# Kernel tuning notes

Measured on AMD Instinct MI355X. Metric: run time of the kernel, lower is better.

Reference implementation:

```python
import jax, jax.numpy as jnp
import numpy as np

H = 1024          # hidden_size
I = 4 * H         # intermediate_size
E = 8             # num routed experts
TOP_K = 2


def setup_inputs() -> dict:
    key = jax.random.key(0)
    ks = jax.random.split(key, 6)
    s = 0.02
    hidden_states = jax.random.normal(ks[0], (4, 4096, H), dtype=jnp.float32)
    # shared expert (num_shared_experts = 1)
    w1_shared = jax.random.normal(ks[1], (H, I), dtype=jnp.float32) * s  # up proj
    w2_shared = jax.random.normal(ks[2], (I, H), dtype=jnp.float32) * s  # down proj
    # routed experts stacked
    w1_routed = jax.random.normal(ks[3], (E, H, I), dtype=jnp.float32) * s
    w2_routed = jax.random.normal(ks[4], (E, I, H), dtype=jnp.float32) * s
    w_router = jax.random.normal(ks[5], (H, E), dtype=jnp.float32) * s
    return {
        "hidden_states": hidden_states,
        "w1_shared": w1_shared,
        "w2_shared": w2_shared,
        "w1_routed": w1_routed,
        "w2_routed": w2_routed,
        "w_router": w_router,
    }


def reference(hidden_states, w1_shared, w2_shared, w1_routed, w2_routed, w_router):
    bsz, seq_len, hidden_dim = hidden_states.shape
    flat = hidden_states.reshape(-1, hidden_dim)              # [T, H]

    # shared expert(s)
    shared_out = jax.nn.silu(flat @ w1_shared) @ w2_shared     # [T, H]

    # router -> softmax -> top-k -> renormalize
    router_logits = flat @ w_router                            # [T, E]
    routing_weights = jax.nn.softmax(router_logits, axis=-1)
    topk_w, topk_idx = jax.lax.top_k(routing_weights, TOP_K)   # [T, K]
    topk_w = topk_w / jnp.sum(topk_w, axis=-1, keepdims=True)

    # combine weights per expert: cw[t, e] = sum_k topk_w[t,k] * (topk_idx[t,k] == e)
    one_hot = jax.nn.one_hot(topk_idx, E, dtype=topk_w.dtype)  # [T, K, E]
    cw = jnp.einsum('tk,tke->te', topk_w, one_hot)             # [T, E]

    # per-expert dense MLP, weighted combine (zero weight == not routed)
    routed_out = jnp.zeros_like(flat)
    for e in range(E):  # fixed small loop over experts
        expert_out = jax.nn.silu(flat @ w1_routed[e]) @ w2_routed[e]  # [T, H]
        routed_out = routed_out + cw[:, e:e + 1] * expert_out

    total = shared_out + routed_out
    return total.reshape(bsz, seq_len, hidden_dim)
```

## Files before the change

kernel.cpp:

```cpp
#include <hip/hip_runtime.h>
#include <cmath>

typedef __bf16 bf16;
typedef bf16 bf16x4 __attribute__((ext_vector_type(4)));
typedef bf16 bf16x8 __attribute__((ext_vector_type(8)));
typedef float f32x4 __attribute__((ext_vector_type(4)));

#define T_TOK 16384
#define HD 1024
#define ID 4096
#define MAXR 51200

__device__ __forceinline__ void async16(const void* g, void* l) {
  void* gp = (void*)g;
  __builtin_amdgcn_global_load_lds((__attribute__((address_space(1))) void*)gp,
                                   (__attribute__((address_space(3))) void*)l,
                                   16, 0, 0);
}

__global__ __launch_bounds__(256)
void cast_x_kernel(const float* __restrict__ X, bf16* __restrict__ Xb) {
  const int i = (blockIdx.x * 256 + threadIdx.x) * 4;
  const float4 v = *(const float4*)(X + i);
  bf16x4 o;
  o.x = (bf16)v.x; o.y = (bf16)v.y; o.z = (bf16)v.z; o.w = (bf16)v.w;
  *(bf16x4*)(Xb + i) = o;
}

__global__ __launch_bounds__(256)
void transpose_cast(const float* __restrict__ srcR, const float* __restrict__ srcS,
                    bf16* __restrict__ dst, int R, int C) {
  const int e = blockIdx.z;
  const float* src = (e < 8) ? srcR + (size_t)e * R * C : srcS;
  __shared__ float tile[64][65];
  const int c0 = blockIdx.x * 64, r0 = blockIdx.y * 64;
  const int tx = threadIdx.x & 15;
  const int ty = threadIdx.x >> 4;
#pragma unroll
  for (int i = 0; i < 64; i += 16) {
    const float4 v = *(const float4*)(src + (size_t)(r0 + ty + i) * C + c0 + tx * 4);
    tile[ty + i][tx * 4 + 0] = v.x;
    tile[ty + i][tx * 4 + 1] = v.y;
    tile[ty + i][tx * 4 + 2] = v.z;
    tile[ty + i][tx * 4 + 3] = v.w;
  }
  __syncthreads();
  bf16* d = dst + (size_t)e * R * C;
#pragma unroll
  for (int i = 0; i < 64; i += 16) {
    const int col = ty + i;
    bf16x4 o;
    o.x = (bf16)tile[tx * 4 + 0][col];
    o.y = (bf16)tile[tx * 4 + 1][col];
    o.z = (bf16)tile[tx * 4 + 2][col];
    o.w = (bf16)tile[tx * 4 + 3][col];
    *(bf16x4*)(d + (size_t)(c0 + col) * R + r0 + tx * 4) = o;
  }
}

__global__ __launch_bounds__(1024)
void router_kernel(const float* __restrict__ X, const float* __restrict__ Wr,
                   int* __restrict__ topk_idx, float* __restrict__ topk_w) {
  __shared__ float W[1024 * 9];
  for (int i = threadIdx.x; i < 1024 * 8; i += 1024)
    W[(i >> 3) * 9 + (i & 7)] = Wr[i];
  __syncthreads();
  const int wave = threadIdx.x >> 6, lane = threadIdx.x & 63;
  const int t = blockIdx.x * 16 + wave;
  const float* xr = X + (size_t)t * HD;
  float acc[8] = {0.f, 0.f, 0.f, 0.f, 0.f, 0.f, 0.f, 0.f};
  for (int j = 0; j < 16; ++j) {
    const float x = xr[lane + j * 64];
    const float* wp = &W[(lane + j * 64) * 9];
#pragma unroll
    for (int e2 = 0; e2 < 8; ++e2) acc[e2] += x * wp[e2];
  }
#pragma unroll
  for (int off = 32; off; off >>= 1)
#pragma unroll
    for (int e2 = 0; e2 < 8; ++e2) acc[e2] += __shfl_down(acc[e2], off);
  if (lane == 0) {
    int i0 = 0; float m0 = acc[0];
#pragma unroll
    for (int e2 = 1; e2 < 8; ++e2) if (acc[e2] > m0) { m0 = acc[e2]; i0 = e2; }
    int i1 = -1; float m1 = -3.4e38f;
#pragma unroll
    for (int e2 = 0; e2 < 8; ++e2)
      if (e2 != i0 && acc[e2] > m1) { m1 = acc[e2]; i1 = e2; }
    const float w0 = 1.f / (1.f + __expf(m1 - m0));
    topk_idx[2 * t] = i0;  topk_idx[2 * t + 1] = i1;
    topk_w[2 * t] = w0;    topk_w[2 * t + 1] = 1.f - w0;
  }
}

__global__ __launch_bounds__(256)
void scatter_kernel(const int* __restrict__ topk_idx, const float* __restrict__ topk_w,
                    int* __restrict__ row_token, float* __restrict__ row_w,
                    int* __restrict__ row_exp, int* __restrict__ token_rows,
                    int* __restrict__ meta) {
  const int e = blockIdx.x;
  const int tid = threadIdx.x;
  __shared__ int hist[8];
  if (tid < 8) hist[tid] = 0;
  __syncthreads();
  for (int t = tid; t < T_TOK; t += 256) {
    atomicAdd(&hist[topk_idx[2 * t]], 1);
    atomicAdd(&hist[topk_idx[2 * t + 1]], 1);
  }
  __syncthreads();

  if (e == 8) {
    for (int r = tid; r < T_TOK; r += 256) {
      row_token[r] = r; row_w[r] = 1.f; row_exp[r] = 8;
    }
    if (tid == 0) {
      int tot = T_TOK;
      for (int i = 0; i < 8; ++i) tot += (hist[i] + 255) & ~255;
      meta[0] = tot;
    }
    return;
  }

  int base = T_TOK;
  for (int i = 0; i < e; ++i) base += (hist[i] + 255) & ~255;
  const int cnt = hist[e];
  const int pc = (cnt + 255) & ~255;

  __shared__ int wsum[4];
  const int wv = tid >> 6, ln = tid & 63;
  int written = 0;
  for (int c = 0; c < T_TOK / 256; ++c) {
    const int t = c * 256 + tid;
    const int i0 = topk_idx[2 * t], i1 = topk_idx[2 * t + 1];
    const int slot = (i0 == e) ? 0 : ((i1 == e) ? 1 : -1);
    const unsigned long long m = __ballot(slot >= 0);
    if (ln == 0) wsum[wv] = (int)__popcll(m);
    __syncthreads();
    int off = written;
    for (int i = 0; i < wv; ++i) off += wsum[i];
    if (slot >= 0) {
      const int rank = (int)__popcll(m & ((1ULL << ln) - 1ULL));
      const int pos = base + off + rank;
      row_token[pos] = t;
      row_w[pos] = topk_w[2 * t + slot];
      row_exp[pos] = e;
      token_rows[2 * t + slot] = pos;
    }
    written += wsum[0] + wsum[1] + wsum[2] + wsum[3];
    __syncthreads();
  }
  for (int p = written + tid; p < pc; p += 256) {
    row_token[base + p] = 0; row_w[base + p] = 0.f; row_exp[base + p] = e;
  }
}

template <int MODE, int NDIM, int KDIM>
__global__ __launch_bounds__(512)
void gemm8(const bf16* __restrict__ A0, const bf16* __restrict__ WT,
           bf16* __restrict__ bout, float* __restrict__ out,
           const int* __restrict__ row_token, const float* __restrict__ row_w,
           const int* __restrict__ row_exp, const int* __restrict__ meta,
           int range_start, int chunk_base) {
  constexpr int NT = KDIM / 32;
  const int total = meta[0];

  const int gx = gridDim.x;
  const int nwg = gx * gridDim.y;
  int id = blockIdx.y * gx + blockIdx.x;
  {
    const int q = nwg >> 3, rm = nwg & 7;
    const int xcd = id & 7, loc = id >> 3;
    id = (xcd < rm ? xcd * (q + 1) : rm * (q + 1) + (xcd - rm) * q) + loc;
  }
  const int bx = id % gx, by = id / gx;

  const int r0 = range_start + by * 256;
  if (r0 >= total) return;
  const int n0 = bx * 256;

  __shared__ __align__(16) char lds[3 * 32768];

  const int tid = threadIdx.x;
  const int wid = tid >> 6, lane = tid & 63;
  const int e = row_exp[r0];
  const bf16* W = WT + (size_t)e * NDIM * KDIM;

  const int tr = tid >> 2;
  const int tb = tid & 3;
  const int rA0 = tr, rA1 = tr + 128;
  const int bl0 = tb ^ ((rA0 >> 1) & 3);
  const int bl1 = tb ^ ((rA1 >> 1) & 3);
  const bf16 *gA0, *gA1;
  if (MODE == 0) {
    gA0 = A0 + (size_t)row_token[r0 + rA0] * KDIM + bl0 * 8;
    gA1 = A0 + (size_t)row_token[r0 + rA1] * KDIM + bl1 * 8;
  } else {
    gA0 = A0 + (size_t)(r0 - chunk_base + rA0) * KDIM + bl0 * 8;
    gA1 = A0 + (size_t)(r0 - chunk_base + rA1) * KDIM + bl1 * 8;
  }
  const bf16* gB0 = W + (size_t)(n0 + rA0) * KDIM + bl0 * 8;
  const bf16* gB1 = W + (size_t)(n0 + rA1) * KDIM + bl1 * 8;
  char* const ldsb = lds;
  const int wo = wid * 1024;

#define STAGE_A0(c, kt) async16(gA0 + (kt) * 32, ldsb + (c) * 32768 + wo)
#define STAGE_A1(c, kt) async16(gA1 + (kt) * 32, ldsb + (c) * 32768 + 8192 + wo)
#define STAGE_B0(c, kt) async16(gB0 + (kt) * 32, ldsb + (c) * 32768 + 16384 + wo)
#define STAGE_B1(c, kt) async16(gB1 + (kt) * 32, ldsb + (c) * 32768 + 24576 + wo)

  const int l15 = lane & 15, kg = lane >> 4;
  const int wr = wid >> 2, wc = wid & 3;
  int offA[8], offB[4];
#pragma unroll
  for (int m = 0; m < 8; ++m) {
    const int row = wr * 128 + m * 16 + l15;
    offA[m] = row * 64 + ((kg ^ ((row >> 1) & 3)) << 4);
  }
#pragma unroll
  for (int n = 0; n < 4; ++n) {
    const int row = wc * 64 + n * 16 + l15;
    offB[n] = 16384 + row * 64 + ((kg ^ ((row >> 1) & 3)) << 4);
  }

  f32x4 acc[8][4] = {};

  STAGE_A0(0, 0); STAGE_A1(0, 0); STAGE_B0(0, 0); STAGE_B1(0, 0);
  STAGE_A0(1, 1); STAGE_A1(1, 1); STAGE_B0(1, 1); STAGE_B1(1, 1);

  int cb = 0, cn = 2;
  for (int kt = 0; kt < NT; ++kt) {
    if (kt + 1 < NT) asm volatile("s_waitcnt vmcnt(4)" ::: "memory");
    else             asm volatile("s_waitcnt vmcnt(0)" ::: "memory");
    __builtin_amdgcn_s_barrier();
    asm volatile("" ::: "memory");
    __builtin_amdgcn_sched_barrier(0);
    const char* Tb = ldsb + cb * 32768;
    const bool pf = (kt + 2 < NT);
    const int k2 = kt + 2;
    bf16x8 bfr[4];
#pragma unroll
    for (int q = 0; q < 4; ++q) {
      if (pf) {
        if (q == 0)      STAGE_A0(cn, k2);
        else if (q == 1) STAGE_A1(cn, k2);
        else if (q == 2) STAGE_B0(cn, k2);
        else             STAGE_B1(cn, k2);
      }
      if (q == 0) {
#pragma unroll
        for (int n = 0; n < 4; ++n) bfr[n] = *(const bf16x8*)(Tb + offB[n]);
      }
      const bf16x8 a0 = *(const bf16x8*)(Tb + offA[2 * q]);
      const bf16x8 a1 = *(const bf16x8*)(Tb + offA[2 * q + 1]);
      __builtin_amdgcn_s_setprio(1);
#pragma unroll
      for (int n = 0; n < 4; ++n) {
        acc[2 * q][n] =
            __builtin_amdgcn_mfma_f32_16x16x32_bf16(a0, bfr[n], acc[2 * q][n], 0, 0, 0);
        acc[2 * q + 1][n] =
            __builtin_amdgcn_mfma_f32_16x16x32_bf16(a1, bfr[n], acc[2 * q + 1][n], 0, 0, 0);
      }
      __builtin_amdgcn_s_setprio(0);
    }
    cb = (cb == 2) ? 0 : cb + 1;
    cn = (cn == 2) ? 0 : cn + 1;
  }
#undef STAGE_A0
#undef STAGE_A1
#undef STAGE_B0
#undef STAGE_B1

  const int orow = wr * 128;
  const int ocol = n0 + wc * 64;
  if (MODE == 0) {
#pragma unroll
    for (int m = 0; m < 8; ++m) {
#pragma unroll
      for (int rr = 0; rr < 4; ++rr) {
        const int row = (r0 - chunk_base) + orow + m * 16 + kg * 4 + rr;
        bf16* p = bout + (size_t)row * NDIM + ocol + l15;
#pragma unroll
        for (int n = 0; n < 4; ++n) {
          const float x = acc[m][n][rr];
          p[n * 16] = (bf16)(x / (1.f + __expf(-x)));
        }
      }
    }
  } else if (e == 8) {
#pragma unroll
    for (int m = 0; m < 8; ++m) {
#pragma unroll
      for (int rr = 0; rr < 4; ++rr) {
        const int row = r0 + orow + m * 16 + kg * 4 + rr;
        const int tok = row_token[row];
        float* p = out + (size_t)tok * HD + ocol + l15;
#pragma unroll
        for (int n = 0; n < 4; ++n) p[n * 16] = acc[m][n][rr];
      }
    }
  } else {
#pragma unroll
    for (int m = 0; m < 8; ++m) {
#pragma unroll
      for (int rr = 0; rr < 4; ++rr) {
        const int row = r0 + orow + m * 16 + kg * 4 + rr;
        const float w = row_w[row];
        bf16* p = bout + (size_t)(row - T_TOK) * HD + ocol + l15;
#pragma unroll
        for (int n = 0; n < 4; ++n) p[n * 16] = (bf16)(w * acc[m][n][rr]);
      }
    }
  }
}

__global__ __launch_bounds__(256)
void combine_kernel(float* __restrict__ out, const bf16* __restrict__ routed_out,
                    const int* __restrict__ token_rows) {
  const int t = blockIdx.x;
  const int i = threadIdx.x * 4;
  const int rA = token_rows[2 * t] - T_TOK;
  const int rB = token_rows[2 * t + 1] - T_TOK;
  float4 o = *(const float4*)(out + (size_t)t * HD + i);
  const bf16x4 a = *(const bf16x4*)(routed_out + (size_t)rA * HD + i);
  const bf16x4 b = *(const bf16x4*)(routed_out + (size_t)rB * HD + i);
  o.x += (float)a.x + (float)b.x;
  o.y += (float)a.y + (float)b.y;
  o.z += (float)a.z + (float)b.z;
  o.w += (float)a.w + (float)b.w;
  *(float4*)(out + (size_t)t * HD + i) = o;
}

extern "C" void kernel_launch(void* const* d_in, const int* in_sizes, int n_in,
                              void* d_out, int out_size, void* d_ws, size_t ws_size,
                              hipStream_t stream) {
  const float* X   = (const float*)d_in[0];
  const float* w1s = (const float*)d_in[1];
  const float* w2s = (const float*)d_in[2];
  const float* w1r = (const float*)d_in[3];
  const float* w2r = (const float*)d_in[4];
  const float* wr  = (const float*)d_in[5];
  float* out = (float*)d_out;

  char* ws = (char*)d_ws;
  bf16* W1T       = (bf16*)(ws + 0);
  bf16* W2T       = (bf16*)(ws + 75497472);
  bf16* Xbf       = (bf16*)(ws + 150994944);
  int* topk_idx   = (int*)(ws + 184549376);
  float* topk_w   = (float*)(ws + 184680448);
  int* row_token  = (int*)(ws + 184811520);
  float* row_w    = (float*)(ws + 185016320);
  int* row_exp    = (int*)(ws + 185221120);
  int* token_rows = (int*)(ws + 185425920);
  int* meta       = (int*)(ws + 185556992);
  bf16* routed_out= (bf16*)(ws + 185557248);
  bf16* act       = (bf16*)(ws + 256860416);

  const size_t avail = ws_size - 256860416ULL;
  long long rc = (long long)(avail / (ID * 2));
  if (rc > MAXR) rc = MAXR;
  rc &= ~255LL;
  if (rc < 256) rc = 256;
  const int Rc = (int)rc;

  cast_x_kernel<<<T_TOK * HD / (256 * 4), 256, 0, stream>>>(X, Xbf);
  transpose_cast<<<dim3(ID / 64, HD / 64, 9), 256, 0, stream>>>(w1r, w1s, W1T, HD, ID);
  transpose_cast<<<dim3(HD / 64, ID / 64, 9), 256, 0, stream>>>(w2r, w2s, W2T, ID, HD);
  router_kernel<<<T_TOK / 16, 1024, 0, stream>>>(X, wr, topk_idx, topk_w);
  scatter_kernel<<<9, 256, 0, stream>>>(topk_idx, topk_w, row_token, row_w,
                                        row_exp, token_rows, meta);

  for (int cb = 0; cb < MAXR; cb += Rc) {
    const int ce = (cb + Rc < MAXR) ? cb + Rc : MAXR;
    gemm8<0, ID, HD><<<dim3(ID / 256, (ce - cb) / 256), 512, 0, stream>>>(
        Xbf, W1T, act, nullptr, row_token, row_w, row_exp, meta, cb, cb);
    gemm8<1, HD, ID><<<dim3(HD / 256, (ce - cb) / 256), 512, 0, stream>>>(
        act, W2T, routed_out, out, row_token, row_w, row_exp, meta, cb, cb);
  }
  combine_kernel<<<T_TOK, 256, 0, stream>>>(out, routed_out, token_rows);
}
```

Baseline: 1.258 ms.

## Fuse cast with router, widen scatter, deepen GEMM pipeline to four stages

Merges the X fp32-to-bf16 cast into the router kernel so X is read once, and uses vectorized float4 loads. The scatter kernel moves to 1024 threads and replaces LDS atomics with per-wave register counts reduced by shuffles. The GEMM goes from a 3-buffer to a 4-buffer LDS ring with prefetch distance 3, which needs 128KB of LDS per block and may reduce occupancy.

```diff
diff --git a/kernel.cpp b/kernel.cpp
--- a/kernel.cpp
+++ b/kernel.cpp
@@ -18,13 +18,50 @@
                                    16, 0, 0);
 }
 
-__global__ __launch_bounds__(256)
-void cast_x_kernel(const float* __restrict__ X, bf16* __restrict__ Xb) {
-  const int i = (blockIdx.x * 256 + threadIdx.x) * 4;
-  const float4 v = *(const float4*)(X + i);
-  bf16x4 o;
-  o.x = (bf16)v.x; o.y = (bf16)v.y; o.z = (bf16)v.z; o.w = (bf16)v.w;
-  *(bf16x4*)(Xb + i) = o;
+__global__ __launch_bounds__(1024)
+void cast_router_kernel(const float* __restrict__ X, const float* __restrict__ Wr,
+                        bf16* __restrict__ Xb, int* __restrict__ topk_idx,
+                        float* __restrict__ topk_w) {
+  __shared__ float W[1024 * 9];
+  for (int i = threadIdx.x; i < 1024 * 8; i += 1024)
+    W[(i >> 3) * 9 + (i & 7)] = Wr[i];
+  __syncthreads();
+  const int wave = threadIdx.x >> 6, lane = threadIdx.x & 63;
+  const int t = blockIdx.x * 16 + wave;
+  const float* xr = X + (size_t)t * HD;
+  bf16* xb = Xb + (size_t)t * HD;
+  float acc[8] = {0.f, 0.f, 0.f, 0.f, 0.f, 0.f, 0.f, 0.f};
+#pragma unroll
+  for (int j = 0; j < 4; ++j) {
+    const int base = lane * 4 + j * 256;
+    const float4 v = *(const float4*)(xr + base);
+    bf16x4 o;
+    o.x = (bf16)v.x; o.y = (bf16)v.y; o.z = (bf16)v.z; o.w = (bf16)v.w;
+    *(bf16x4*)(xb + base) = o;
+    const float xv[4] = {v.x, v.y, v.z, v.w};
+#pragma unroll
+    for (int c = 0; c < 4; ++c) {
+      const float* wp = &W[(base + c) * 9];
+#pragma unroll
+      for (int e2 = 0; e2 < 8; ++e2) acc[e2] += xv[c] * wp[e2];
+    }
+  }
+#pragma unroll
+  for (int off = 32; off; off >>= 1)
+#pragma unroll
+    for (int e2 = 0; e2 < 8; ++e2) acc[e2] += __shfl_down(acc[e2], off);
+  if (lane == 0) {
+    int i0 = 0; float m0 = acc[0];
+#pragma unroll
+    for (int e2 = 1; e2 < 8; ++e2) if (acc[e2] > m0) { m0 = acc[e2]; i0 = e2; }
+    int i1 = -1; float m1 = -3.4e38f;
+#pragma unroll
+    for (int e2 = 0; e2 < 8; ++e2)
+      if (e2 != i0 && acc[e2] > m1) { m1 = acc[e2]; i1 = e2; }
+    const float w0 = 1.f / (1.f + __expf(m1 - m0));
+    topk_idx[2 * t] = i0;  topk_idx[2 * t + 1] = i1;
+    topk_w[2 * t] = w0;    topk_w[2 * t + 1] = 1.f - w0;
+  }
 }
 
 __global__ __launch_bounds__(256)
@@ -59,58 +96,46 @@
 }
 
 __global__ __launch_bounds__(1024)
-void router_kernel(const float* __restrict__ X, const float* __restrict__ Wr,
-                   int* __restrict__ topk_idx, float* __restrict__ topk_w) {
-  __shared__ float W[1024 * 9];
-  for (int i = threadIdx.x; i < 1024 * 8; i += 1024)
-    W[(i >> 3) * 9 + (i & 7)] = Wr[i];
-  __syncthreads();
-  const int wave = threadIdx.x >> 6, lane = threadIdx.x & 63;
-  const int t = blockIdx.x * 16 + wave;
-  const float* xr = X + (size_t)t * HD;
-  float acc[8] = {0.f, 0.f, 0.f, 0.f, 0.f, 0.f, 0.f, 0.f};
-  for (int j = 0; j < 16; ++j) {
-    const float x = xr[lane + j * 64];
-    const float* wp = &W[(lane + j * 64) * 9];
-#pragma unroll
-    for (int e2 = 0; e2 < 8; ++e2) acc[e2] += x * wp[e2];
-  }
-#pragma unroll
-  for (int off = 32; off; off >>= 1)
-#pragma unroll
-    for (int e2 = 0; e2 < 8; ++e2) acc[e2] += __shfl_down(acc[e2], off);
-  if (lane == 0) {
-    int i0 = 0; float m0 = acc[0];
-#pragma unroll
-    for (int e2 = 1; e2 < 8; ++e2) if (acc[e2] > m0) { m0 = acc[e2]; i0 = e2; }
-    int i1 = -1; float m1 = -3.4e38f;
-#pragma unroll
-    for (int e2 = 0; e2 < 8; ++e2)
-      if (e2 != i0 && acc[e2] > m1) { m1 = acc[e2]; i1 = e2; }
-    const float w0 = 1.f / (1.f + __expf(m1 - m0));
-    topk_idx[2 * t] = i0;  topk_idx[2 * t + 1] = i1;
-    topk_w[2 * t] = w0;    topk_w[2 * t + 1] = 1.f - w0;
-  }
-}
-
-__global__ __launch_bounds__(256)
 void scatter_kernel(const int* __restrict__ topk_idx, const float* __restrict__ topk_w,
                     int* __restrict__ row_token, float* __restrict__ row_w,
                     int* __restrict__ row_exp, int* __restrict__ token_rows,
                     int* __restrict__ meta) {
   const int e = blockIdx.x;
   const int tid = threadIdx.x;
+  const int wv = tid >> 6, ln = tid & 63;
+  __shared__ int whist[16][8];
   __shared__ int hist[8];
-  if (tid < 8) hist[tid] = 0;
+
+  int lc0 = 0, lc1 = 0, lc2 = 0, lc3 = 0, lc4 = 0, lc5 = 0, lc6 = 0, lc7 = 0;
+  for (int t = tid; t < T_TOK; t += 1024) {
+    const int i0 = topk_idx[2 * t], i1 = topk_idx[2 * t + 1];
+    lc0 += (i0 == 0) + (i1 == 0);  lc1 += (i0 == 1) + (i1 == 1);
+    lc2 += (i0 == 2) + (i1 == 2);  lc3 += (i0 == 3) + (i1 == 3);
+    lc4 += (i0 == 4) + (i1 == 4);  lc5 += (i0 == 5) + (i1 == 5);
+    lc6 += (i0 == 6) + (i1 == 6);  lc7 += (i0 == 7) + (i1 == 7);
+  }
+#pragma unroll
+  for (int off = 32; off; off >>= 1) {
+    lc0 += __shfl_down(lc0, off); lc1 += __shfl_down(lc1, off);
+    lc2 += __shfl_down(lc2, off); lc3 += __shfl_down(lc3, off);
+    lc4 += __shfl_down(lc4, off); lc5 += __shfl_down(lc5, off);
+    lc6 += __shfl_down(lc6, off); lc7 += __shfl_down(lc7, off);
+  }
+  if (ln == 0) {
+    whist[wv][0] = lc0; whist[wv][1] = lc1; whist[wv][2] = lc2; whist[wv][3] = lc3;
+    whist[wv][4] = lc4; whist[wv][5] = lc5; whist[wv][6] = lc6; whist[wv][7] = lc7;
+  }
   __syncthreads();
-  for (int t = tid; t < T_TOK; t += 256) {
-    atomicAdd(&hist[topk_idx[2 * t]], 1);
-    atomicAdd(&hist[topk_idx[2 * t + 1]], 1);
+  if (tid < 8) {
+    int s = 0;
+#pragma unroll
+    for (int w = 0; w < 16; ++w) s += whist[w][tid];
+    hist[tid] = s;
   }
   __syncthreads();
 
   if (e == 8) {
-    for (int r = tid; r < T_TOK; r += 256) {
+    for (int r = tid; r < T_TOK; r += 1024) {
       row_token[r] = r; row_w[r] = 1.f; row_exp[r] = 8;
     }
     if (tid == 0) {
@@ -126,11 +151,10 @@
   const int cnt = hist[e];
   const int pc = (cnt + 255) & ~255;
 
-  __shared__ int wsum[4];
-  const int wv = tid >> 6, ln = tid & 63;
+  __shared__ int wsum[16];
   int written = 0;
-  for (int c = 0; c < T_TOK / 256; ++c) {
-    const int t = c * 256 + tid;
+  for (int c = 0; c < T_TOK / 1024; ++c) {
+    const int t = c * 1024 + tid;
     const int i0 = topk_idx[2 * t], i1 = topk_idx[2 * t + 1];
     const int slot = (i0 == e) ? 0 : ((i1 == e) ? 1 : -1);
     const unsigned long long m = __ballot(slot >= 0);
@@ -146,10 +170,13 @@
       row_exp[pos] = e;
       token_rows[2 * t + slot] = pos;
     }
-    written += wsum[0] + wsum[1] + wsum[2] + wsum[3];
+    int tot = 0;
+#pragma unroll
+    for (int i = 0; i < 16; ++i) tot += wsum[i];
+    written += tot;
     __syncthreads();
   }
-  for (int p = written + tid; p < pc; p += 256) {
+  for (int p = written + tid; p < pc; p += 1024) {
     row_token[base + p] = 0; row_w[base + p] = 0.f; row_exp[base + p] = e;
   }
 }
@@ -178,7 +205,7 @@
   if (r0 >= total) return;
   const int n0 = bx * 256;
 
-  __shared__ __align__(16) char lds[3 * 32768];
+  __shared__ __align__(16) char lds[4 * 32768];
 
   const int tid = threadIdx.x;
   const int wid = tid >> 6, lane = tid & 63;
@@ -226,25 +253,28 @@
 
   STAGE_A0(0, 0); STAGE_A1(0, 0); STAGE_B0(0, 0); STAGE_B1(0, 0);
   STAGE_A0(1, 1); STAGE_A1(1, 1); STAGE_B0(1, 1); STAGE_B1(1, 1);
-
-  int cb = 0, cn = 2;
+  STAGE_A0(2, 2); STAGE_A1(2, 2); STAGE_B0(2, 2); STAGE_B1(2, 2);
+
   for (int kt = 0; kt < NT; ++kt) {
-    if (kt + 1 < NT) asm volatile("s_waitcnt vmcnt(4)" ::: "memory");
-    else             asm volatile("s_waitcnt vmcnt(0)" ::: "memory");
+    const int rem = NT - 1 - kt;
+    if (rem >= 2)      asm volatile("s_waitcnt vmcnt(8)" ::: "memory");
+    else if (rem == 1) asm volatile("s_waitcnt vmcnt(4)" ::: "memory");
+    else               asm volatile("s_waitcnt vmcnt(0)" ::: "memory");
     __builtin_amdgcn_s_barrier();
     asm volatile("" ::: "memory");
     __builtin_amdgcn_sched_barrier(0);
-    const char* Tb = ldsb + cb * 32768;
-    const bool pf = (kt + 2 < NT);
-    const int k2 = kt + 2;
+    const char* Tb = ldsb + (kt & 3) * 32768;
+    const bool pf = (kt + 3 < NT);
+    const int k3 = kt + 3;
+    const int cn = (kt + 3) & 3;
     bf16x8 bfr[4];
 #pragma unroll
     for (int q = 0; q < 4; ++q) {
       if (pf) {
-        if (q == 0)      STAGE_A0(cn, k2);
-        else if (q == 1) STAGE_A1(cn, k2);
-        else if (q == 2) STAGE_B0(cn, k2);
-        else             STAGE_B1(cn, k2);
+        if (q == 0)      STAGE_A0(cn, k3);
+        else if (q == 1) STAGE_A1(cn, k3);
+        else if (q == 2) STAGE_B0(cn, k3);
+        else             STAGE_B1(cn, k3);
       }
       if (q == 0) {
 #pragma unroll
@@ -262,8 +292,6 @@
       }
       __builtin_amdgcn_s_setprio(0);
     }
-    cb = (cb == 2) ? 0 : cb + 1;
-    cn = (cn == 2) ? 0 : cn + 1;
   }
 #undef STAGE_A0
 #undef STAGE_A1
@@ -362,12 +390,11 @@
   if (rc < 256) rc = 256;
   const int Rc = (int)rc;
 
-  cast_x_kernel<<<T_TOK * HD / (256 * 4), 256, 0, stream>>>(X, Xbf);
+  cast_router_kernel<<<T_TOK / 16, 1024, 0, stream>>>(X, wr, Xbf, topk_idx, topk_w);
   transpose_cast<<<dim3(ID / 64, HD / 64, 9), 256, 0, stream>>>(w1r, w1s, W1T, HD, ID);
   transpose_cast<<<dim3(HD / 64, ID / 64, 9), 256, 0, stream>>>(w2r, w2s, W2T, ID, HD);
-  router_kernel<<<T_TOK / 16, 1024, 0, stream>>>(X, wr, topk_idx, topk_w);
-  scatter_kernel<<<9, 256, 0, stream>>>(topk_idx, topk_w, row_token, row_w,
-                                        row_exp, token_rows, meta);
+  scatter_kernel<<<9, 1024, 0, stream>>>(topk_idx, topk_w, row_token, row_w,
+                                         row_exp, token_rows, meta);
 
   for (int cb = 0; cb < MAXR; cb += Rc) {
     const int ce = (cb + Rc < MAXR) ? cb + Rc : MAXR;
```

New measurement: 1.244 ms. No clear change (-1.1%).
